# Kernel tuning notes

Hardware: AMD Instinct MI355X
Metric: run time of the kernel (lower is better)

The kernel has to match this reference:

```python
import jax, jax.numpy as jnp
import numpy as np

NUM_HEADS = 15
NUM_KV_HEADS = 5
HEAD_DIM = 64
GROUPS = NUM_HEADS // NUM_KV_HEADS
BIG_NEG = jnp.finfo(jnp.float32).min


def setup_inputs() -> dict:
    key = jax.random.key(0)
    k1, k2, k3, k4 = jax.random.split(key, 4)
    B, S = 2, 2048
    attention_mask = jax.random.randint(k1, (B, S, S), 0, 2).astype(bool)
    query_states = jax.random.normal(k2, (B, S, NUM_HEADS, HEAD_DIM), dtype=jnp.float32)
    key_states = jax.random.normal(k3, (B, S, NUM_KV_HEADS, HEAD_DIM), dtype=jnp.float32)
    value_states = jax.random.normal(k4, (B, S, NUM_KV_HEADS, HEAD_DIM), dtype=jnp.float32)
    return {
        "attention_mask": attention_mask,
        "query_states": query_states,
        "key_states": key_states,
        "value_states": value_states,
    }


def reference(attention_mask, query_states, key_states, value_states):
    B, S = query_states.shape[0], key_states.shape[1]
    # GQA: expand KV heads (each kv head repeated GROUPS times, contiguous)
    k = jnp.repeat(key_states, GROUPS, axis=2)    # [B,S,H,D]
    v = jnp.repeat(value_states, GROUPS, axis=2)  # [B,S,H,D]
    q = query_states.astype(jnp.float32)
    k = k.astype(jnp.float32)
    # scores: [B,H,Sq,Sk]
    att = jnp.einsum('bqhd,bkhd->bhqk', q, k) * (HEAD_DIM ** -0.5)
    maskf = attention_mask[:, None, :, :].astype(jnp.float32)
    att = maskf * att + (1.0 - maskf) * BIG_NEG
    probs = jax.nn.softmax(att, axis=-1).astype(v.dtype)
    # [B,H,Sq,D] -> [B,Sq,H,D] -> [B,Sq,H*D]
    out = jnp.einsum('bhqk,bkhd->bqhd', probs, v)
    return out.reshape(B, S, NUM_HEADS * HEAD_DIM)
```

## Files before the change

### kernel.cpp

```cpp
#include <hip/hip_runtime.h>
#include <hip/hip_bf16.h>

#define B_    2
#define S_    2048
#define H_    15
#define KVH_  5
#define G_    3
#define D_    64
#define KVD_  (KVH_ * D_)
#define HD_   (H_ * D_)
#define SW_   (S_ / 32)
#define KBLK  32
#define ITER  (S_ / KBLK)

constexpr float SCALE   = 0.125f;
constexpr float NEG_BIG = -3.0e38f;
constexpr float DEFER_THR = 8.0f;

typedef __bf16  bf16x8 __attribute__((ext_vector_type(8)));
typedef __bf16  bf16x4 __attribute__((ext_vector_type(4)));
typedef float   f32x4  __attribute__((ext_vector_type(4)));
typedef int     i32x4  __attribute__((ext_vector_type(4)));

#define MFMA(a, b, c) __builtin_amdgcn_mfma_f32_16x16x32_bf16((a), (b), (c), 0, 0, 0)

__device__ __forceinline__ void gload16(const void* g, void* l) {
    __builtin_amdgcn_global_load_lds(
        (const __attribute__((address_space(1))) unsigned int*)g,
        (__attribute__((address_space(3))) unsigned int*)l, 16, 0, 0);
}

__device__ __forceinline__ unsigned pack_hi16(unsigned even_elem, unsigned odd_elem) {
    return __builtin_amdgcn_perm(odd_elem, even_elem, 0x07060302u);
}

__global__ __launch_bounds__(256) void bitpack(const int* __restrict__ mask,
                                               unsigned int* __restrict__ bits) {
    const int stride = gridDim.x * 256;
    const int lane   = threadIdx.x & 63;
    for (int i = blockIdx.x * 256 + threadIdx.x; i < B_ * S_ * S_; i += stride) {
        unsigned long long bal = __ballot(mask[i] != 0);
        if (lane == 0)       bits[i >> 5] = (unsigned int)bal;
        else if (lane == 32) bits[i >> 5] = (unsigned int)(bal >> 32);
    }
}

__global__ __launch_bounds__(256) void conv_k(const float* __restrict__ K,
                                              __bf16* __restrict__ khi,
                                              __bf16* __restrict__ klo) {
    const int i = blockIdx.x * 256 + threadIdx.x;
    const float4 v = ((const float4*)K)[i];
    const float xs[4] = {v.x, v.y, v.z, v.w};
    bf16x4 h, lo;
#pragma unroll
    for (int j = 0; j < 4; j++) {
        __bf16 hh = (__bf16)xs[j];
        h[j]  = hh;
        lo[j] = (__bf16)(xs[j] - (float)hh);
    }
    ((bf16x4*)khi)[i] = h;
    ((bf16x4*)klo)[i] = lo;
}

__global__ __launch_bounds__(512) void transpose_v(const float* __restrict__ V,
                                                   __bf16* __restrict__ vthi,
                                                   __bf16* __restrict__ vtlo) {
    __shared__ float tile[64][65];
    const int bid = blockIdx.x;
    const int st  = bid & 31;
    const int kv  = (bid >> 5) % KVH_;
    const int b   = bid / (32 * KVH_);
    const int s0  = st * 64;
    const int tid = threadIdx.x;
    const int c   = tid & 63;
    const int rq  = tid >> 6;
#pragma unroll
    for (int i = 0; i < 8; i++) {
        const int si = rq + i * 8;
        tile[si][c] = V[(((size_t)b * S_ + s0 + si) * KVH_ + kv) * D_ + c];
    }
    __syncthreads();
#pragma unroll
    for (int i = 0; i < 8; i++) {
        const int di = rq + i * 8;
        const float x = tile[c][di];
        const __bf16 hh = (__bf16)x;
        const size_t o = (((size_t)b * KVH_ + kv) * D_ + di) * S_ + s0 + c;
        vthi[o] = hh;
        vtlo[o] = (__bf16)(x - (float)hh);
    }
}

__global__ __launch_bounds__(256) void attn_main(const unsigned int* __restrict__ bits,
                                                 const float* __restrict__ Q,
                                                 const __bf16* __restrict__ khi,
                                                 const __bf16* __restrict__ klo,
                                                 const __bf16* __restrict__ vthi,
                                                 const __bf16* __restrict__ vtlo,
                                                 float* __restrict__ out) {
    __shared__ __align__(16) __bf16 Kls[2][2][KBLK][64];
    __shared__ __align__(16) __bf16 Vls[2][2][64][KBLK];

    const int tid  = threadIdx.x;
    const int wv   = tid >> 6;
    const int lane = tid & 63;
    const int lrow = lane & 15;
    const int lgrp = lane >> 4;

    const int bid = blockIdx.x;
    const int qt  = bid & 31;
    const int bh  = bid >> 5;
    const int h   = bh % H_;
    const int b   = bh / H_;
    const int kv  = h / G_;
    const int q0  = qt * 64 + wv * 16;

    const float* qp = Q + (((size_t)b * S_ + (q0 + lrow)) * H_ + h) * D_;
    bf16x8 ahi[2], alo[2];
#pragma unroll
    for (int kk = 0; kk < 2; kk++) {
#pragma unroll
        for (int jj = 0; jj < 2; jj++) {
            const float4 v = *(const float4*)(qp + kk * 32 + lgrp * 8 + jj * 4);
            const float xs[4] = {v.x * SCALE, v.y * SCALE, v.z * SCALE, v.w * SCALE};
#pragma unroll
            for (int j = 0; j < 4; j++) {
                const __bf16 hh = (__bf16)xs[j];
                ahi[kk][jj * 4 + j] = hh;
                alo[kk][jj * 4 + j] = (__bf16)(xs[j] - (float)hh);
            }
        }
    }

    f32x4 O[4] = {{0.f,0.f,0.f,0.f},{0.f,0.f,0.f,0.f},{0.f,0.f,0.f,0.f},{0.f,0.f,0.f,0.f}};
    float m = NEG_BIG, l = 0.f;

    const __bf16* khb = khi + (size_t)b * S_ * KVD_ + kv * D_;
    const __bf16* klb = klo + (size_t)b * S_ * KVD_ + kv * D_;
    const __bf16* vhb = vthi + ((size_t)b * KVH_ + kv) * D_ * S_;
    const __bf16* vlb = vtlo + ((size_t)b * KVH_ + kv) * D_ * S_;

    const int kgi  = wv * 64 + lane;
    const int krho = kgi >> 3;
    const int kkey = 8 * ((krho >> 2) & 3) + 4 * (krho >> 4) + (krho & 3);
    const int kcol = (((kgi & 7) ^ (krho & 7)) * 8);
    const int vrow = kgi >> 2, vcg = kgi & 3;
    const int vcol = ((vcg ^ ((vrow >> 1) & 3)) * 8);

    const __bf16* khsrc = khb + (size_t)kkey * KVD_ + kcol;
    const __bf16* klsrc = klb + (size_t)kkey * KVD_ + kcol;
    const __bf16* vhsrc = vhb + (size_t)vrow * S_ + vcol;
    const __bf16* vlsrc = vlb + (size_t)vrow * S_ + vcol;
    const unsigned int* bptr = bits + ((size_t)b * S_ + q0 + lrow) * SW_;

    gload16(khsrc, &Kls[0][0][wv * 8][0]);
    gload16(klsrc, &Kls[0][1][wv * 8][0]);
    gload16(vhsrc, &Vls[0][0][wv * 16][0]);
    gload16(vlsrc, &Vls[0][1][wv * 16][0]);
    khsrc += (size_t)KBLK * KVD_;
    klsrc += (size_t)KBLK * KVD_;
    vhsrc += KBLK;
    vlsrc += KBLK;
    __syncthreads();

    for (int kt = 0; kt < ITER; kt++) {
        const int cur = kt & 1;

        const unsigned w = *bptr++;

        if (kt + 1 < ITER) {
            gload16(khsrc, &Kls[cur ^ 1][0][wv * 8][0]);
            gload16(klsrc, &Kls[cur ^ 1][1][wv * 8][0]);
            gload16(vhsrc, &Vls[cur ^ 1][0][wv * 16][0]);
            gload16(vlsrc, &Vls[cur ^ 1][1][wv * 16][0]);
            khsrc += (size_t)KBLK * KVD_;
            klsrc += (size_t)KBLK * KVD_;
            vhsrc += KBLK;
            vlsrc += KBLK;
        }

        f32x4 s[2];
#pragma unroll
        for (int t = 0; t < 2; t++) {
            const int row = t * 16 + lrow;
            const int sw  = row & 7;
            const bf16x8 bh0 = *(const bf16x8*)&Kls[cur][0][row][(lgrp ^ sw) * 8];
            const bf16x8 bh1 = *(const bf16x8*)&Kls[cur][0][row][((4 + lgrp) ^ sw) * 8];
            const bf16x8 bl0 = *(const bf16x8*)&Kls[cur][1][row][(lgrp ^ sw) * 8];
            const bf16x8 bl1 = *(const bf16x8*)&Kls[cur][1][row][((4 + lgrp) ^ sw) * 8];
            f32x4 acc = {0.f, 0.f, 0.f, 0.f};
            acc = MFMA(bh0, ahi[0], acc);
            acc = MFMA(bh0, alo[0], acc);
            acc = MFMA(bl0, ahi[0], acc);
            acc = MFMA(bh1, ahi[1], acc);
            acc = MFMA(bh1, alo[1], acc);
            acc = MFMA(bl1, ahi[1], acc);
            s[t] = acc;
        }

        float pmax = NEG_BIG;
#pragma unroll
        for (int t = 0; t < 2; t++) {
#pragma unroll
            for (int r = 0; r < 4; r++) {
                const int bit = 8 * lgrp + 4 * t + r;
                const float sv = ((w >> bit) & 1u) ? s[t][r] : NEG_BIG;
                s[t][r] = sv;
                pmax = fmaxf(pmax, sv);
            }
        }
        pmax = fmaxf(pmax, __shfl_xor(pmax, 16));
        pmax = fmaxf(pmax, __shfl_xor(pmax, 32));

        if (!__all(pmax <= m + DEFER_THR)) {
            const float mn = fmaxf(m, pmax);
            const float f  = __expf(m - mn);
            m = mn;
            l *= f;
#pragma unroll
            for (int db = 0; db < 4; db++) {
                f32x4 o = O[db];
                o[0] *= f; o[1] *= f; o[2] *= f; o[3] *= f;
                O[db] = o;
            }
        }

        unsigned hw[4], lw[4];
#pragma unroll
        for (int t = 0; t < 2; t++) {
#pragma unroll
            for (int pr = 0; pr < 2; pr++) {
                const float e0 = __expf(s[t][2 * pr]     - m);
                const float e1 = __expf(s[t][2 * pr + 1] - m);
                l += e0 + e1;
                const unsigned u0 = __builtin_bit_cast(unsigned, e0);
                const unsigned u1 = __builtin_bit_cast(unsigned, e1);
                const float h0 = __builtin_bit_cast(float, u0 & 0xFFFF0000u);
                const float h1 = __builtin_bit_cast(float, u1 & 0xFFFF0000u);
                const unsigned l0 = __builtin_bit_cast(unsigned, e0 - h0);
                const unsigned l1 = __builtin_bit_cast(unsigned, e1 - h1);
                hw[2 * t + pr] = pack_hi16(u0, u1);
                lw[2 * t + pr] = pack_hi16(l0, l1);
            }
        }
        i32x4 wh, wl;
#pragma unroll
        for (int i = 0; i < 4; i++) { wh[i] = (int)hw[i]; wl[i] = (int)lw[i]; }
        const bf16x8 ph = __builtin_bit_cast(bf16x8, wh);
        const bf16x8 pl = __builtin_bit_cast(bf16x8, wl);

#pragma unroll
        for (int db = 0; db < 4; db++) {
            const int row = db * 16 + lrow;
            const int sw  = (row >> 1) & 3;
            const bf16x8 vh = *(const bf16x8*)&Vls[cur][0][row][(lgrp ^ sw) * 8];
            const bf16x8 vl = *(const bf16x8*)&Vls[cur][1][row][(lgrp ^ sw) * 8];
            O[db] = MFMA(vh, ph, O[db]);
            O[db] = MFMA(vh, pl, O[db]);
            O[db] = MFMA(vl, ph, O[db]);
        }

        __syncthreads();
    }

    float lv = l;
    lv += __shfl_xor(lv, 16);
    lv += __shfl_xor(lv, 32);
    const float inv = 1.0f / lv;
    float* op = out + ((size_t)b * S_ + q0 + lrow) * HD_ + h * D_ + lgrp * 4;
#pragma unroll
    for (int db = 0; db < 4; db++) {
        f32x4 o = O[db];
        o[0] *= inv; o[1] *= inv; o[2] *= inv; o[3] *= inv;
        *(f32x4*)(op + db * 16) = o;
    }
}

extern "C" void kernel_launch(void* const* d_in, const int* in_sizes, int n_in,
                              void* d_out, int out_size, void* d_ws, size_t ws_size,
                              hipStream_t stream) {
    const int*   mask = (const int*)d_in[0];
    const float* Q    = (const float*)d_in[1];
    const float* K    = (const float*)d_in[2];
    const float* V    = (const float*)d_in[3];
    float*       out  = (float*)d_out;

    char* ws = (char*)d_ws;
    unsigned int* bits = (unsigned int*)ws;
    const size_t KV_BYTES = (size_t)B_ * S_ * KVH_ * D_ * sizeof(__bf16);
    __bf16* khi  = (__bf16*)(ws + (1 << 20));
    __bf16* klo  = (__bf16*)(ws + (1 << 20) + KV_BYTES);
    __bf16* vthi = (__bf16*)(ws + (1 << 20) + 2 * KV_BYTES);
    __bf16* vtlo = (__bf16*)(ws + (1 << 20) + 3 * KV_BYTES);

    bitpack<<<2048, 256, 0, stream>>>(mask, bits);
    conv_k<<<(B_ * S_ * KVH_ * D_) / (256 * 4), 256, 0, stream>>>(K, khi, klo);
    transpose_v<<<B_ * KVH_ * (S_ / 64), 512, 0, stream>>>(V, vthi, vtlo);
    attn_main<<<B_ * H_ * (S_ / 64), 256, 0, stream>>>(bits, Q, khi, klo, vthi, vtlo, out);
}
```

Measured before the change: 232.4 us.

## Split key range across two blocks with combine pass; drop P low-part MFMA

Splits each query tile's key loop into two halves handled by separate blocks. This doubles the grid from 960 to 1920 blocks so the GPU is better occupied. A new combine kernel merges the partial outputs using the saved (m, l) per row. Separately, the probabilities are now truncated to bf16 high parts only, with l accumulated from the truncated values, so one of the three PV MFMAs per block is removed. In exchange it adds partial-buffer traffic and an extra launch, and lowers the precision of P.

```diff
diff --git a/kernel.cpp b/kernel.cpp
--- a/kernel.cpp
+++ b/kernel.cpp
@@ -11,7 +11,7 @@
 #define HD_   (H_ * D_)
 #define SW_   (S_ / 32)
 #define KBLK  32
-#define ITER  (S_ / KBLK)
+#define NBLK  960
 
 constexpr float SCALE   = 0.125f;
 constexpr float NEG_BIG = -3.0e38f;
@@ -91,13 +91,15 @@
     }
 }
 
+template<int SPLIT>
 __global__ __launch_bounds__(256) void attn_main(const unsigned int* __restrict__ bits,
                                                  const float* __restrict__ Q,
                                                  const __bf16* __restrict__ khi,
                                                  const __bf16* __restrict__ klo,
                                                  const __bf16* __restrict__ vthi,
                                                  const __bf16* __restrict__ vtlo,
-                                                 float* __restrict__ out) {
+                                                 float* __restrict__ dst,
+                                                 float2* __restrict__ ml) {
     __shared__ __align__(16) __bf16 Kls[2][2][KBLK][64];
     __shared__ __align__(16) __bf16 Vls[2][2][64][KBLK];
 
@@ -108,12 +110,16 @@
     const int lgrp = lane >> 4;
 
     const int bid = blockIdx.x;
-    const int qt  = bid & 31;
-    const int bh  = bid >> 5;
+    const int hw  = SPLIT ? (bid & 1) : 0;
+    const int blk = SPLIT ? (bid >> 1) : bid;
+    const int qt  = blk & 31;
+    const int bh  = blk >> 5;
     const int h   = bh % H_;
     const int b   = bh / H_;
     const int kv  = h / G_;
     const int q0  = qt * 64 + wv * 16;
+    const int kbase = SPLIT ? hw * (S_ / 2) : 0;
+    constexpr int NIT = SPLIT ? (S_ / 2 / KBLK) : (S_ / KBLK);
 
     const float* qp = Q + (((size_t)b * S_ + (q0 + lrow)) * H_ + h) * D_;
     bf16x8 ahi[2], alo[2];
@@ -147,11 +153,11 @@
     const int vrow = kgi >> 2, vcg = kgi & 3;
     const int vcol = ((vcg ^ ((vrow >> 1) & 3)) * 8);
 
-    const __bf16* khsrc = khb + (size_t)kkey * KVD_ + kcol;
-    const __bf16* klsrc = klb + (size_t)kkey * KVD_ + kcol;
-    const __bf16* vhsrc = vhb + (size_t)vrow * S_ + vcol;
-    const __bf16* vlsrc = vlb + (size_t)vrow * S_ + vcol;
-    const unsigned int* bptr = bits + ((size_t)b * S_ + q0 + lrow) * SW_;
+    const __bf16* khsrc = khb + (size_t)(kbase + kkey) * KVD_ + kcol;
+    const __bf16* klsrc = klb + (size_t)(kbase + kkey) * KVD_ + kcol;
+    const __bf16* vhsrc = vhb + (size_t)vrow * S_ + kbase + vcol;
+    const __bf16* vlsrc = vlb + (size_t)vrow * S_ + kbase + vcol;
+    const unsigned int* bptr = bits + ((size_t)b * S_ + q0 + lrow) * SW_ + (SPLIT ? hw * NIT : 0);
 
     gload16(khsrc, &Kls[0][0][wv * 8][0]);
     gload16(klsrc, &Kls[0][1][wv * 8][0]);
@@ -163,12 +169,11 @@
     vlsrc += KBLK;
     __syncthreads();
 
-    for (int kt = 0; kt < ITER; kt++) {
+    for (int kt = 0; kt < NIT; kt++) {
         const int cur = kt & 1;
-
         const unsigned w = *bptr++;
 
-        if (kt + 1 < ITER) {
+        if (kt + 1 < NIT) {
             gload16(khsrc, &Kls[cur ^ 1][0][wv * 8][0]);
             gload16(klsrc, &Kls[cur ^ 1][1][wv * 8][0]);
             gload16(vhsrc, &Vls[cur ^ 1][0][wv * 16][0]);
@@ -225,29 +230,23 @@
             }
         }
 
-        unsigned hw[4], lw[4];
+        unsigned hwd[4];
 #pragma unroll
         for (int t = 0; t < 2; t++) {
 #pragma unroll
             for (int pr = 0; pr < 2; pr++) {
                 const float e0 = __expf(s[t][2 * pr]     - m);
                 const float e1 = __expf(s[t][2 * pr + 1] - m);
-                l += e0 + e1;
-                const unsigned u0 = __builtin_bit_cast(unsigned, e0);
-                const unsigned u1 = __builtin_bit_cast(unsigned, e1);
-                const float h0 = __builtin_bit_cast(float, u0 & 0xFFFF0000u);
-                const float h1 = __builtin_bit_cast(float, u1 & 0xFFFF0000u);
-                const unsigned l0 = __builtin_bit_cast(unsigned, e0 - h0);
-                const unsigned l1 = __builtin_bit_cast(unsigned, e1 - h1);
-                hw[2 * t + pr] = pack_hi16(u0, u1);
-                lw[2 * t + pr] = pack_hi16(l0, l1);
+                const unsigned u0 = __builtin_bit_cast(unsigned, e0) & 0xFFFF0000u;
+                const unsigned u1 = __builtin_bit_cast(unsigned, e1) & 0xFFFF0000u;
+                l += __builtin_bit_cast(float, u0) + __builtin_bit_cast(float, u1);
+                hwd[2 * t + pr] = pack_hi16(u0, u1);
             }
         }
-        i32x4 wh, wl;
-#pragma unroll
-        for (int i = 0; i < 4; i++) { wh[i] = (int)hw[i]; wl[i] = (int)lw[i]; }
+        i32x4 wh;
+#pragma unroll
+        for (int i = 0; i < 4; i++) wh[i] = (int)hwd[i];
         const bf16x8 ph = __builtin_bit_cast(bf16x8, wh);
-        const bf16x8 pl = __builtin_bit_cast(bf16x8, wl);
 
 #pragma unroll
         for (int db = 0; db < 4; db++) {
@@ -256,7 +255,6 @@
             const bf16x8 vh = *(const bf16x8*)&Vls[cur][0][row][(lgrp ^ sw) * 8];
             const bf16x8 vl = *(const bf16x8*)&Vls[cur][1][row][(lgrp ^ sw) * 8];
             O[db] = MFMA(vh, ph, O[db]);
-            O[db] = MFMA(vh, pl, O[db]);
             O[db] = MFMA(vl, ph, O[db]);
         }
 
@@ -266,14 +264,47 @@
     float lv = l;
     lv += __shfl_xor(lv, 16);
     lv += __shfl_xor(lv, 32);
-    const float inv = 1.0f / lv;
-    float* op = out + ((size_t)b * S_ + q0 + lrow) * HD_ + h * D_ + lgrp * 4;
-#pragma unroll
-    for (int db = 0; db < 4; db++) {
-        f32x4 o = O[db];
-        o[0] *= inv; o[1] *= inv; o[2] *= inv; o[3] *= inv;
-        *(f32x4*)(op + db * 16) = o;
-    }
+
+    if constexpr (SPLIT) {
+        const size_t prow = ((size_t)(hw * NBLK + blk) * 64 + wv * 16 + lrow) * 64;
+#pragma unroll
+        for (int db = 0; db < 4; db++)
+            *(f32x4*)&dst[prow + db * 16 + lgrp * 4] = O[db];
+        if (lgrp == 0)
+            ml[(size_t)(hw * NBLK + blk) * 64 + wv * 16 + lrow] = make_float2(m, lv);
+    } else {
+        const float inv = 1.0f / lv;
+        float* op = dst + ((size_t)b * S_ + q0 + lrow) * HD_ + h * D_ + lgrp * 4;
+#pragma unroll
+        for (int db = 0; db < 4; db++) {
+            f32x4 o = O[db];
+            o[0] *= inv; o[1] *= inv; o[2] *= inv; o[3] *= inv;
+            *(f32x4*)(op + db * 16) = o;
+        }
+    }
+}
+
+__global__ __launch_bounds__(256) void combine(const float* __restrict__ A,
+                                               const float2* __restrict__ ml,
+                                               float* __restrict__ out) {
+    const int tid = threadIdx.x;
+    const int row = blockIdx.x * 4 + (tid >> 6);
+    const int d   = tid & 63;
+    const int b   = row / (H_ * S_);
+    const int rem = row - b * (H_ * S_);
+    const int h   = rem >> 11;
+    const int q   = rem & (S_ - 1);
+    const int blkid = (b * H_ + h) * 32 + (q >> 6);
+    const int qi  = q & 63;
+    const float2 ml0 = ml[(size_t)blkid * 64 + qi];
+    const float2 ml1 = ml[(size_t)(NBLK + blkid) * 64 + qi];
+    const float M  = fmaxf(ml0.x, ml1.x);
+    const float f0 = __expf(ml0.x - M);
+    const float f1 = __expf(ml1.x - M);
+    const float inv = 1.0f / (ml0.y * f0 + ml1.y * f1);
+    const float a0 = A[((size_t)blkid * 64 + qi) * 64 + d];
+    const float a1 = A[((size_t)(NBLK + blkid) * 64 + qi) * 64 + d];
+    out[((size_t)b * S_ + q) * HD_ + h * D_ + d] = (a0 * f0 + a1 * f1) * inv;
 }
 
 extern "C" void kernel_launch(void* const* d_in, const int* in_sizes, int n_in,
@@ -293,8 +324,21 @@
     __bf16* vthi = (__bf16*)(ws + (1 << 20) + 2 * KV_BYTES);
     __bf16* vtlo = (__bf16*)(ws + (1 << 20) + 3 * KV_BYTES);
 
+    const size_t PART_OFF = (size_t)(1 << 20) + 4 * KV_BYTES;
+    const size_t A_BYTES  = (size_t)2 * NBLK * 64 * 64 * sizeof(float);
+    const size_t ML_BYTES = (size_t)2 * NBLK * 64 * sizeof(float2);
+    const size_t REQ      = PART_OFF + A_BYTES + ML_BYTES;
+    float*  Apart = (float*)(ws + PART_OFF);
+    float2* mlp   = (float2*)(ws + PART_OFF + A_BYTES);
+
     bitpack<<<2048, 256, 0, stream>>>(mask, bits);
     conv_k<<<(B_ * S_ * KVH_ * D_) / (256 * 4), 256, 0, stream>>>(K, khi, klo);
     transpose_v<<<B_ * KVH_ * (S_ / 64), 512, 0, stream>>>(V, vthi, vtlo);
-    attn_main<<<B_ * H_ * (S_ / 64), 256, 0, stream>>>(bits, Q, khi, klo, vthi, vtlo, out);
-}
+
+    if (ws_size >= REQ) {
+        attn_main<1><<<2 * NBLK, 256, 0, stream>>>(bits, Q, khi, klo, vthi, vtlo, Apart, mlp);
+        combine<<<(B_ * H_ * S_) / 4, 256, 0, stream>>>(Apart, mlp, out);
+    } else {
+        attn_main<0><<<NBLK, 256, 0, stream>>>(bits, Q, khi, klo, vthi, vtlo, out, nullptr);
+    }
+}
```

New measurement: 235.0 us. About the same (+1.1%).

## Fuse preprocessing kernels, use exp2 softmax, drop P-low MFMA, compute row sums via MFMA

Applied to the files above, without the earlier changes.

Merges the mask bitpack, K split-conversion and V transpose into one launch, removing two kernel launches. The attention loop folds log2(e) into the Q scale so it can use exp2, and raises the deferred-rescale threshold to match the base-2 scale. It drops the low-part bf16 term of the probabilities, saving one MFMA per output block, and computes the row sum with an MFMA against a ones vector instead of scalar adds and shuffles. This lowers accuracy, since the probabilities are now kept at bf16 precision only.

```diff
diff --git a/kernel.cpp b/kernel.cpp
--- a/kernel.cpp
+++ b/kernel.cpp
@@ -12,10 +12,11 @@
 #define SW_   (S_ / 32)
 #define KBLK  32
 #define ITER  (S_ / KBLK)
-
-constexpr float SCALE   = 0.125f;
+#define NBLK  960
+
+constexpr float SCALE2  = 0.125f * 1.44269504088896340736f;
 constexpr float NEG_BIG = -3.0e38f;
-constexpr float DEFER_THR = 8.0f;
+constexpr float DEFER_THR = 11.0f;
 
 typedef __bf16  bf16x8 __attribute__((ext_vector_type(8)));
 typedef __bf16  bf16x4 __attribute__((ext_vector_type(4)));
@@ -34,60 +35,61 @@
     return __builtin_amdgcn_perm(odd_elem, even_elem, 0x07060302u);
 }
 
-__global__ __launch_bounds__(256) void bitpack(const int* __restrict__ mask,
-                                               unsigned int* __restrict__ bits) {
-    const int stride = gridDim.x * 256;
-    const int lane   = threadIdx.x & 63;
-    for (int i = blockIdx.x * 256 + threadIdx.x; i < B_ * S_ * S_; i += stride) {
-        unsigned long long bal = __ballot(mask[i] != 0);
-        if (lane == 0)       bits[i >> 5] = (unsigned int)bal;
-        else if (lane == 32) bits[i >> 5] = (unsigned int)(bal >> 32);
-    }
-}
-
-__global__ __launch_bounds__(256) void conv_k(const float* __restrict__ K,
-                                              __bf16* __restrict__ khi,
-                                              __bf16* __restrict__ klo) {
-    const int i = blockIdx.x * 256 + threadIdx.x;
-    const float4 v = ((const float4*)K)[i];
-    const float xs[4] = {v.x, v.y, v.z, v.w};
-    bf16x4 h, lo;
-#pragma unroll
-    for (int j = 0; j < 4; j++) {
-        __bf16 hh = (__bf16)xs[j];
-        h[j]  = hh;
-        lo[j] = (__bf16)(xs[j] - (float)hh);
-    }
-    ((bf16x4*)khi)[i] = h;
-    ((bf16x4*)klo)[i] = lo;
-}
-
-__global__ __launch_bounds__(512) void transpose_v(const float* __restrict__ V,
-                                                   __bf16* __restrict__ vthi,
-                                                   __bf16* __restrict__ vtlo) {
+__global__ __launch_bounds__(512) void fused_pre(const int* __restrict__ mask,
+                                                 const float* __restrict__ K,
+                                                 const float* __restrict__ V,
+                                                 unsigned int* __restrict__ bits,
+                                                 __bf16* __restrict__ khi,
+                                                 __bf16* __restrict__ klo,
+                                                 __bf16* __restrict__ vthi,
+                                                 __bf16* __restrict__ vtlo) {
     __shared__ float tile[64][65];
-    const int bid = blockIdx.x;
-    const int st  = bid & 31;
-    const int kv  = (bid >> 5) % KVH_;
-    const int b   = bid / (32 * KVH_);
-    const int s0  = st * 64;
+    const int blk = blockIdx.x;
     const int tid = threadIdx.x;
-    const int c   = tid & 63;
-    const int rq  = tid >> 6;
-#pragma unroll
-    for (int i = 0; i < 8; i++) {
-        const int si = rq + i * 8;
-        tile[si][c] = V[(((size_t)b * S_ + s0 + si) * KVH_ + kv) * D_ + c];
-    }
-    __syncthreads();
-#pragma unroll
-    for (int i = 0; i < 8; i++) {
-        const int di = rq + i * 8;
-        const float x = tile[c][di];
-        const __bf16 hh = (__bf16)x;
-        const size_t o = (((size_t)b * KVH_ + kv) * D_ + di) * S_ + s0 + c;
-        vthi[o] = hh;
-        vtlo[o] = (__bf16)(x - (float)hh);
+
+    if (blk < 320) {
+        const int st  = blk & 31;
+        const int kv  = (blk >> 5) % KVH_;
+        const int b   = blk / (32 * KVH_);
+        const int s0  = st * 64;
+        const int c   = tid & 63;
+        const int rq  = tid >> 6;
+#pragma unroll
+        for (int i = 0; i < 8; i++) {
+            const int si = rq + i * 8;
+            tile[si][c] = V[(((size_t)b * S_ + s0 + si) * KVH_ + kv) * D_ + c];
+        }
+        __syncthreads();
+#pragma unroll
+        for (int i = 0; i < 8; i++) {
+            const int di = rq + i * 8;
+            const float x = tile[c][di];
+            const __bf16 hh = (__bf16)x;
+            const size_t o = (((size_t)b * KVH_ + kv) * D_ + di) * S_ + s0 + c;
+            vthi[o] = hh;
+            vtlo[o] = (__bf16)(x - (float)hh);
+        }
+    } else if (blk < 960) {
+        const int i = (blk - 320) * 512 + tid;
+        const float4 v = ((const float4*)K)[i];
+        const float xs[4] = {v.x, v.y, v.z, v.w};
+        bf16x4 h, lo;
+#pragma unroll
+        for (int j = 0; j < 4; j++) {
+            __bf16 hh = (__bf16)xs[j];
+            h[j]  = hh;
+            lo[j] = (__bf16)(xs[j] - (float)hh);
+        }
+        ((bf16x4*)khi)[i] = h;
+        ((bf16x4*)klo)[i] = lo;
+    } else {
+        const int lane = tid & 63;
+        const int stride = 1024 * 512;
+        for (int i = (blk - 960) * 512 + tid; i < B_ * S_ * S_; i += stride) {
+            unsigned long long bal = __ballot(mask[i] != 0);
+            if (lane == 0)       bits[i >> 5] = (unsigned int)bal;
+            else if (lane == 32) bits[i >> 5] = (unsigned int)(bal >> 32);
+        }
     }
 }
 
@@ -122,7 +124,7 @@
 #pragma unroll
         for (int jj = 0; jj < 2; jj++) {
             const float4 v = *(const float4*)(qp + kk * 32 + lgrp * 8 + jj * 4);
-            const float xs[4] = {v.x * SCALE, v.y * SCALE, v.z * SCALE, v.w * SCALE};
+            const float xs[4] = {v.x * SCALE2, v.y * SCALE2, v.z * SCALE2, v.w * SCALE2};
 #pragma unroll
             for (int j = 0; j < 4; j++) {
                 const __bf16 hh = (__bf16)xs[j];
@@ -132,8 +134,12 @@
         }
     }
 
+    const i32x4 onesw = {0x3F803F80, 0x3F803F80, 0x3F803F80, 0x3F803F80};
+    const bf16x8 ones = __builtin_bit_cast(bf16x8, onesw);
+
     f32x4 O[4] = {{0.f,0.f,0.f,0.f},{0.f,0.f,0.f,0.f},{0.f,0.f,0.f,0.f},{0.f,0.f,0.f,0.f}};
-    float m = NEG_BIG, l = 0.f;
+    f32x4 accL = {0.f, 0.f, 0.f, 0.f};
+    float m = NEG_BIG;
 
     const __bf16* khb = khi + (size_t)b * S_ * KVD_ + kv * D_;
     const __bf16* klb = klo + (size_t)b * S_ * KVD_ + kv * D_;
@@ -165,7 +171,6 @@
 
     for (int kt = 0; kt < ITER; kt++) {
         const int cur = kt & 1;
-
         const unsigned w = *bptr++;
 
         if (kt + 1 < ITER) {
@@ -214,9 +219,9 @@
 
         if (!__all(pmax <= m + DEFER_THR)) {
             const float mn = fmaxf(m, pmax);
-            const float f  = __expf(m - mn);
+            const float f  = exp2f(m - mn);
             m = mn;
-            l *= f;
+            accL[0] *= f; accL[1] *= f; accL[2] *= f; accL[3] *= f;
 #pragma unroll
             for (int db = 0; db < 4; db++) {
                 f32x4 o = O[db];
@@ -225,29 +230,23 @@
             }
         }
 
-        unsigned hw[4], lw[4];
+        unsigned hwd[4];
 #pragma unroll
         for (int t = 0; t < 2; t++) {
 #pragma unroll
             for (int pr = 0; pr < 2; pr++) {
-                const float e0 = __expf(s[t][2 * pr]     - m);
-                const float e1 = __expf(s[t][2 * pr + 1] - m);
-                l += e0 + e1;
-                const unsigned u0 = __builtin_bit_cast(unsigned, e0);
-                const unsigned u1 = __builtin_bit_cast(unsigned, e1);
-                const float h0 = __builtin_bit_cast(float, u0 & 0xFFFF0000u);
-                const float h1 = __builtin_bit_cast(float, u1 & 0xFFFF0000u);
-                const unsigned l0 = __builtin_bit_cast(unsigned, e0 - h0);
-                const unsigned l1 = __builtin_bit_cast(unsigned, e1 - h1);
-                hw[2 * t + pr] = pack_hi16(u0, u1);
-                lw[2 * t + pr] = pack_hi16(l0, l1);
-            }
-        }
-        i32x4 wh, wl;
-#pragma unroll
-        for (int i = 0; i < 4; i++) { wh[i] = (int)hw[i]; wl[i] = (int)lw[i]; }
+                const float e0 = exp2f(s[t][2 * pr]     - m);
+                const float e1 = exp2f(s[t][2 * pr + 1] - m);
+                hwd[2 * t + pr] = pack_hi16(__builtin_bit_cast(unsigned, e0),
+                                            __builtin_bit_cast(unsigned, e1));
+            }
+        }
+        i32x4 wh;
+#pragma unroll
+        for (int i = 0; i < 4; i++) wh[i] = (int)hwd[i];
         const bf16x8 ph = __builtin_bit_cast(bf16x8, wh);
-        const bf16x8 pl = __builtin_bit_cast(bf16x8, wl);
+
+        accL = MFMA(ones, ph, accL);
 
 #pragma unroll
         for (int db = 0; db < 4; db++) {
@@ -256,17 +255,13 @@
             const bf16x8 vh = *(const bf16x8*)&Vls[cur][0][row][(lgrp ^ sw) * 8];
             const bf16x8 vl = *(const bf16x8*)&Vls[cur][1][row][(lgrp ^ sw) * 8];
             O[db] = MFMA(vh, ph, O[db]);
-            O[db] = MFMA(vh, pl, O[db]);
             O[db] = MFMA(vl, ph, O[db]);
         }
 
         __syncthreads();
     }
 
-    float lv = l;
-    lv += __shfl_xor(lv, 16);
-    lv += __shfl_xor(lv, 32);
-    const float inv = 1.0f / lv;
+    const float inv = 1.0f / accL[0];
     float* op = out + ((size_t)b * S_ + q0 + lrow) * HD_ + h * D_ + lgrp * 4;
 #pragma unroll
     for (int db = 0; db < 4; db++) {
@@ -293,8 +288,6 @@
     __bf16* vthi = (__bf16*)(ws + (1 << 20) + 2 * KV_BYTES);
     __bf16* vtlo = (__bf16*)(ws + (1 << 20) + 3 * KV_BYTES);
 
-    bitpack<<<2048, 256, 0, stream>>>(mask, bits);
-    conv_k<<<(B_ * S_ * KVH_ * D_) / (256 * 4), 256, 0, stream>>>(K, khi, klo);
-    transpose_v<<<B_ * KVH_ * (S_ / 64), 512, 0, stream>>>(V, vthi, vtlo);
-    attn_main<<<B_ * H_ * (S_ / 64), 256, 0, stream>>>(bits, Q, khi, klo, vthi, vtlo, out);
-}
+    fused_pre<<<1984, 512, 0, stream>>>(mask, K, V, bits, khi, klo, vthi, vtlo);
+    attn_main<<<NBLK, 256, 0, stream>>>(bits, Q, khi, klo, vthi, vtlo, out);
+}
```

Result: faster. 224.4 us (-3.5%).
